# Kernel tuning notes

Measured on AMD Instinct MI355X. Metric: run time of the kernel, lower is better.

Reference implementation:

```python
import jax, jax.numpy as jnp
import numpy as np


def setup_inputs() -> dict:
    key = jax.random.key(0)
    ks = jax.random.split(key, 7)
    B, T, D_in, H, D_out = 512, 1024, 128, 512, 128
    s = lambda k, shp, fan: jax.random.normal(k, shp, jnp.float32) / np.sqrt(fan)
    return {
        "x": jax.random.normal(ks[0], (B, T, D_in), jnp.float32),
        "Wx": s(ks[1], (H, D_in), D_in),
        "bx": jnp.zeros((H,), jnp.float32),
        "Wh": s(ks[2], (H, H), H),
        "bh": jnp.zeros((H,), jnp.float32),
        "Wy": s(ks[3], (D_out, H), H),
        "by": jnp.zeros((D_out,), jnp.float32),
    }


def reference(x, Wx, bx, Wh, bh, Wy, by):
    # x: [B, T, D_in]. Hoist input projection into one big GEMM (same math).
    B, T, _ = x.shape
    H = Wh.shape[0]
    xp = jnp.einsum("btd,hd->bth", x, Wx) + bx + bh  # [B, T, H]

    def step(h, xp_t):
        h = jnp.tanh(xp_t + h @ Wh.T)
        return h, None

    h0 = jnp.zeros((B, H), x.dtype)
    h_T, _ = jax.lax.scan(step, h0, jnp.swapaxes(xp, 0, 1))  # scan over time
    y = h_T @ Wy.T + by  # [B, D_out]
    return y
```

## Files before the change

### kernel.cpp

```cpp
#include <hip/hip_runtime.h>

typedef __bf16 bf16x8 __attribute__((ext_vector_type(8)));
typedef unsigned short ushort8_t __attribute__((ext_vector_type(8)));
typedef float f32x4 __attribute__((ext_vector_type(4)));
typedef unsigned int uint4_t __attribute__((ext_vector_type(4)));

#define MFMA16(a,b,c) __builtin_amdgcn_mfma_f32_16x16x32_bf16((a),(b),(c),0,0,0)


__device__ __forceinline__ unsigned short f2bf(float f) {
  unsigned int u = __float_as_uint(f);
  u += 0x7FFFu + ((u >> 16) & 1u);
  return (unsigned short)(u >> 16);
}

__device__ __forceinline__ bf16x8 pack8(const float* __restrict__ s) {
  ushort8_t u;
#pragma unroll
  for (int j = 0; j < 8; ++j) u[j] = f2bf(s[j]);
  return __builtin_bit_cast(bf16x8, u);
}

__global__ void rnn_prep(const float* __restrict__ Wx, const float* __restrict__ bx,
                         const float* __restrict__ Wh, const float* __restrict__ bh,
                         void* __restrict__ ws) {
  int gid = blockIdx.x * 256 + threadIdx.x;
  if (blockIdx.x < 72) {
    int l = gid & 63;
    int f = (gid >> 6) % 18;
    int w = gid / (64 * 18);
    int nt = f & 1, fi = f >> 1;
    int n = w * 32 + nt * 16 + (l & 15);
    int kg = l >> 4;
    const float* src;
    if (fi < 5) src = Wh + (size_t)n * 512 + (11 + fi) * 32 + kg * 8;
    else        src = Wx + (size_t)n * 128 + (fi - 5) * 32 + kg * 8;
    ushort8_t u;
#pragma unroll
    for (int j = 0; j < 8; ++j) u[j] = f2bf(src[j]);
    ((ushort8_t*)ws)[gid] = u;
  } else {
    int i = (gid - 72 * 256) * 2;
    float* bias = (float*)((char*)ws + 294912);
    bias[i]     = bx[i] + bh[i];
    bias[i + 1] = bx[i + 1] + bh[i + 1];
  }
}

__global__ __launch_bounds__(1024) void rnn_scan(
    const float* __restrict__ x, const float* __restrict__ Wh,
    const float* __restrict__ Wy, const float* __restrict__ by,
    const void* __restrict__ ws, float* __restrict__ out) {
  __shared__ alignas(16) char h_lds[32768];
  __shared__ alignas(16) char x_lds[8192];

  const int tid = threadIdx.x;
  const int w = tid >> 6, l = tid & 63;
  const int m = l & 15, kg = l >> 4;
  const int sw = (m & 7) << 4;
  const int bb = blockIdx.x << 4;

  const int hE = m * 1024 + ((kg * 16) ^ sw);
  const int hO = m * 1024 + ((64 + kg * 16) ^ sw);
  const int xE = m * 256 + ((kg * 16) ^ sw);
  const int xO = m * 256 + ((64 + kg * 16) ^ sw);

  const float* xrow = x + (size_t)(bb + w) * (1024 * 128) + 2 * l;
  const int k2 = 2 * l;
  const int xw_off = w * 256 + ((k2 >> 6) << 7) + ((2 * (k2 & 63)) ^ ((w & 7) << 4));

  int cblk[2], ca2[2];
#pragma unroll
  for (int nt = 0; nt < 2; ++nt) {
    int c = w * 32 + nt * 16 + m;
    cblk[nt] = (c >> 6) << 7;
    ca2[nt] = 2 * (c & 63);
  }

  const float* bias = (const float*)((const char*)ws + 294912);
  const float b0 = bias[w * 32 + m];
  const float b1 = bias[w * 32 + 16 + m];

  bf16x8 bres[22];
#pragma unroll
  for (int kt = 0; kt < 11; ++kt)
#pragma unroll
    for (int nt = 0; nt < 2; ++nt)
      bres[kt * 2 + nt] = pack8(Wh + (size_t)(w * 32 + nt * 16 + m) * 512 + kt * 32 + kg * 8);

  const bf16x8* sp = (const bf16x8*)ws + (w * 18) * 64 + l;

  *(uint4_t*)(h_lds + tid * 16) = (uint4_t){0, 0, 0, 0};
  {
    float2 xv = *(const float2*)(xrow);
    unsigned int p = (unsigned)f2bf(xv.x) | ((unsigned)f2bf(xv.y) << 16);
    *(unsigned int*)(x_lds + xw_off) = p;
  }
  __syncthreads();

  for (int t = 0; t < 1024; ++t) {
    const int cur = t & 1, nxt = cur ^ 1;
    const char* hb = h_lds + cur * 16384;
    const char* xb = x_lds + cur * 4096;

    unsigned long long spi = (unsigned long long)sp;
    asm volatile("" : "+v"(spi));
    const bf16x8* spv = (const bf16x8*)spi;

    const int tt = (t < 1023) ? t + 1 : 1023;
    float2 xv = *(const float2*)(xrow + (size_t)tt * 128);

    f32x4 acc0 = {0.f, 0.f, 0.f, 0.f}, acc1 = {0.f, 0.f, 0.f, 0.f};

#pragma unroll
    for (int kt = 0; kt < 11; ++kt) {
      bf16x8 a = *(const bf16x8*)(hb + ((kt & 1) ? hO : hE) + (kt >> 1) * 128);
      acc0 = MFMA16(a, bres[kt * 2], acc0);
      acc1 = MFMA16(a, bres[kt * 2 + 1], acc1);
    }
#pragma unroll
    for (int fi = 0; fi < 9; ++fi) {
      const int kt = 11 + fi;
      bf16x8 sb0 = spv[(fi * 2) * 64];
      bf16x8 sb1 = spv[(fi * 2 + 1) * 64];
      bf16x8 a;
      if (kt < 16) {
        a = *(const bf16x8*)(hb + ((kt & 1) ? hO : hE) + (kt >> 1) * 128);
      } else {
        const int kx = kt - 16;
        a = *(const bf16x8*)(xb + ((kx & 1) ? xO : xE) + (kx >> 1) * 128);
      }
      acc0 = MFMA16(a, sb0, acc0);
      acc1 = MFMA16(a, sb1, acc1);
    }

    {
      unsigned int p = (unsigned)f2bf(xv.x) | ((unsigned)f2bf(xv.y) << 16);
      *(unsigned int*)(x_lds + nxt * 4096 + xw_off) = p;
    }

    char* hn = h_lds + nxt * 16384;
#pragma unroll
    for (int nt = 0; nt < 2; ++nt) {
      const float bnt = nt ? b1 : b0;
      const f32x4 av = nt ? acc1 : acc0;
#pragma unroll
      for (int i = 0; i < 4; ++i) {
        const int r = kg * 4 + i;
        float pre = av[i] + bnt;
        float e = __expf(2.f * pre);
        float hv = 1.f - 2.f / (e + 1.f);
        const int off = r * 1024 + cblk[nt] + (ca2[nt] ^ ((r & 7) << 4));
        *(unsigned short*)(hn + off) = f2bf(hv);
      }
    }
    __syncthreads();
  }

  if (w < 8) {
    f32x4 aY = {0.f, 0.f, 0.f, 0.f};
#pragma unroll
    for (int kt = 0; kt < 16; ++kt) {
      bf16x8 a = *(const bf16x8*)(h_lds + ((kt & 1) ? hO : hE) + (kt >> 1) * 128);
      bf16x8 b = pack8(Wy + (size_t)(w * 16 + m) * 512 + kt * 32 + kg * 8);
      aY = MFMA16(a, b, aY);
    }
    const float bv = by[w * 16 + m];
#pragma unroll
    for (int i = 0; i < 4; ++i)
      out[(size_t)(bb + kg * 4 + i) * 128 + w * 16 + m] = aY[i] + bv;
  }
}

extern "C" void kernel_launch(void* const* d_in, const int* in_sizes, int n_in,
                              void* d_out, int out_size, void* d_ws, size_t ws_size,
                              hipStream_t stream) {
  const float* x  = (const float*)d_in[0];
  const float* Wx = (const float*)d_in[1];
  const float* bx = (const float*)d_in[2];
  const float* Wh = (const float*)d_in[3];
  const float* bh = (const float*)d_in[4];
  const float* Wy = (const float*)d_in[5];
  const float* by = (const float*)d_in[6];

  rnn_prep<<<73, 256, 0, stream>>>(Wx, bx, Wh, bh, d_ws);
  rnn_scan<<<32, 1024, 0, stream>>>(x, Wh, Wy, by, d_ws, (float*)d_out);
}
```

Measured before the change: 5.133 ms.

## Split each batch group across two cooperating blocks exchanging hidden state via global mailboxes

After: 9.162 ms. 78.5% more time.

```diff
diff --git a/kernel.cpp b/kernel.cpp
--- a/kernel.cpp
+++ b/kernel.cpp
@@ -13,162 +13,204 @@
   u += 0x7FFFu + ((u >> 16) & 1u);
   return (unsigned short)(u >> 16);
 }
-
-__device__ __forceinline__ bf16x8 pack8(const float* __restrict__ s) {
+__device__ __forceinline__ bf16x8 pack8v(float4 a, float4 b) {
   ushort8_t u;
-#pragma unroll
-  for (int j = 0; j < 8; ++j) u[j] = f2bf(s[j]);
+  u[0] = f2bf(a.x); u[1] = f2bf(a.y); u[2] = f2bf(a.z); u[3] = f2bf(a.w);
+  u[4] = f2bf(b.x); u[5] = f2bf(b.y); u[6] = f2bf(b.z); u[7] = f2bf(b.w);
   return __builtin_bit_cast(bf16x8, u);
 }
-
-__global__ void rnn_prep(const float* __restrict__ Wx, const float* __restrict__ bx,
-                         const float* __restrict__ Wh, const float* __restrict__ bh,
+__device__ __forceinline__ bf16x8 pack8p(const float* __restrict__ s) {
+  float4 a = *(const float4*)s, b = *(const float4*)(s + 4);
+  return pack8v(a, b);
+}
+
+__global__ void rnn_prep(const float* __restrict__ bx, const float* __restrict__ bh,
                          void* __restrict__ ws) {
-  int gid = blockIdx.x * 256 + threadIdx.x;
-  if (blockIdx.x < 72) {
-    int l = gid & 63;
-    int f = (gid >> 6) % 18;
-    int w = gid / (64 * 18);
-    int nt = f & 1, fi = f >> 1;
-    int n = w * 32 + nt * 16 + (l & 15);
-    int kg = l >> 4;
-    const float* src;
-    if (fi < 5) src = Wh + (size_t)n * 512 + (11 + fi) * 32 + kg * 8;
-    else        src = Wx + (size_t)n * 128 + (fi - 5) * 32 + kg * 8;
-    ushort8_t u;
-#pragma unroll
-    for (int j = 0; j < 8; ++j) u[j] = f2bf(src[j]);
-    ((ushort8_t*)ws)[gid] = u;
-  } else {
-    int i = (gid - 72 * 256) * 2;
-    float* bias = (float*)((char*)ws + 294912);
-    bias[i]     = bx[i] + bh[i];
-    bias[i + 1] = bx[i + 1] + bh[i + 1];
-  }
-}
-
-__global__ __launch_bounds__(1024) void rnn_scan(
-    const float* __restrict__ x, const float* __restrict__ Wh,
-    const float* __restrict__ Wy, const float* __restrict__ by,
-    const void* __restrict__ ws, float* __restrict__ out) {
+  int tid = threadIdx.x;
+  ((float*)ws)[tid] = bx[tid] + bh[tid];
+  if (tid < 128) *(unsigned*)((char*)ws + 2048 + tid * 64) = 0u;
+}
+
+__global__ __launch_bounds__(256, 1) void rnn_scan(
+    const float* __restrict__ x, const float* __restrict__ Wx,
+    const float* __restrict__ Wh, const float* __restrict__ Wy,
+    const float* __restrict__ by, void* __restrict__ ws,
+    float* __restrict__ out) {
   __shared__ alignas(16) char h_lds[32768];
   __shared__ alignas(16) char x_lds[8192];
 
   const int tid = threadIdx.x;
-  const int w = tid >> 6, l = tid & 63;
-  const int m = l & 15, kg = l >> 4;
+  const int w = tid >> 6, l = tid & 63, m = l & 15, kg = l >> 4;
+  const int g = blockIdx.x & 31, role = blockIdx.x >> 5;
+  const int bb = g << 4;
+  const int pbase = (1 - role) << 8;
   const int sw = (m & 7) << 4;
-  const int bb = blockIdx.x << 4;
-
-  const int hE = m * 1024 + ((kg * 16) ^ sw);
-  const int hO = m * 1024 + ((64 + kg * 16) ^ sw);
-  const int xE = m * 256 + ((kg * 16) ^ sw);
-  const int xO = m * 256 + ((64 + kg * 16) ^ sw);
-
-  const float* xrow = x + (size_t)(bb + w) * (1024 * 128) + 2 * l;
-  const int k2 = 2 * l;
-  const int xw_off = w * 256 + ((k2 >> 6) << 7) + ((2 * (k2 & 63)) ^ ((w & 7) << 4));
-
-  int cblk[2], ca2[2];
-#pragma unroll
-  for (int nt = 0; nt < 2; ++nt) {
-    int c = w * 32 + nt * 16 + m;
-    cblk[nt] = (c >> 6) << 7;
-    ca2[nt] = 2 * (c & 63);
-  }
-
-  const float* bias = (const float*)((const char*)ws + 294912);
-  const float b0 = bias[w * 32 + m];
-  const float b1 = bias[w * 32 + 16 + m];
-
-  bf16x8 bres[22];
-#pragma unroll
-  for (int kt = 0; kt < 11; ++kt)
-#pragma unroll
-    for (int nt = 0; nt < 2; ++nt)
-      bres[kt * 2 + nt] = pack8(Wh + (size_t)(w * 32 + nt * 16 + m) * 512 + kt * 32 + kg * 8);
-
-  const bf16x8* sp = (const bf16x8*)ws + (w * 18) * 64 + l;
-
-  *(uint4_t*)(h_lds + tid * 16) = (uint4_t){0, 0, 0, 0};
+
+  char* wsb = (char*)ws;
+  const float* biasp = (const float*)wsb;
+
+  bf16x8 bw[20][4];
+  float bv[4];
+#pragma unroll
+  for (int nt = 0; nt < 4; ++nt) {
+    const int cn = role * 256 + w * 64 + nt * 16 + m;
+    bv[nt] = biasp[cn];
+#pragma unroll
+    for (int kt = 0; kt < 16; ++kt)
+      bw[kt][nt] = pack8p(Wh + (size_t)cn * 512 + kt * 32 + kg * 8);
+#pragma unroll
+    for (int kx = 0; kx < 4; ++kx)
+      bw[16 + kx][nt] = pack8p(Wx + (size_t)cn * 128 + kx * 32 + kg * 8);
+  }
+
+  int aoff_h[16], aoff_x[4];
+#pragma unroll
+  for (int kt = 0; kt < 16; ++kt)
+    aoff_h[kt] = m * 1024 + ((kt >> 1) << 7) + ((((kt & 1) << 6) + (kg << 4)) ^ sw);
+#pragma unroll
+  for (int kx = 0; kx < 4; ++kx)
+    aoff_x[kx] = m * 256 + ((kx >> 1) << 7) + ((((kx & 1) << 6) + (kg << 4)) ^ sw);
+
+  const int srow = tid >> 4, sk0 = (tid & 15) << 3;
+  const float* xsrc = x + (size_t)(bb + srow) * 1024 * 128 + sk0;
+  const int xw_off = srow * 256 + ((sk0 >> 6) << 7) + (((sk0 & 63) << 1) ^ ((srow & 7) << 4));
+
+  char* const mail_my0 = wsb + 16384 + (size_t)((g * 2 + role) * 2 + 0) * 8192;
+  char* const mail_my1 = wsb + 16384 + (size_t)((g * 2 + role) * 2 + 1) * 8192;
+  const char* const mail_pt0 = wsb + 16384 + (size_t)((g * 2 + (1 - role)) * 2 + 0) * 8192;
+  const char* const mail_pt1 = wsb + 16384 + (size_t)((g * 2 + (1 - role)) * 2 + 1) * 8192;
+  unsigned* const flag_my0 = (unsigned*)(wsb + 2048 + ((g * 2 + role) * 2 + 0) * 64);
+  unsigned* const flag_my1 = (unsigned*)(wsb + 2048 + ((g * 2 + role) * 2 + 1) * 64);
+  const unsigned* const flag_pt0 = (const unsigned*)(wsb + 2048 + ((g * 2 + (1 - role)) * 2 + 0) * 64);
+  const unsigned* const flag_pt1 = (const unsigned*)(wsb + 2048 + ((g * 2 + (1 - role)) * 2 + 1) * 64);
+
   {
-    float2 xv = *(const float2*)(xrow);
-    unsigned int p = (unsigned)f2bf(xv.x) | ((unsigned)f2bf(xv.y) << 16);
-    *(unsigned int*)(x_lds + xw_off) = p;
+    uint4_t z = {0, 0, 0, 0};
+#pragma unroll
+    for (int j = 0; j < 4; ++j) *(uint4_t*)(h_lds + tid * 64 + j * 16) = z;
+    float4 xa = *(const float4*)(xsrc);
+    float4 xb2 = *(const float4*)(xsrc + 4);
+    *(bf16x8*)(x_lds + xw_off) = pack8v(xa, xb2);
   }
   __syncthreads();
 
   for (int t = 0; t < 1024; ++t) {
-    const int cur = t & 1, nxt = cur ^ 1;
-    const char* hb = h_lds + cur * 16384;
-    const char* xb = x_lds + cur * 4096;
-
-    unsigned long long spi = (unsigned long long)sp;
-    asm volatile("" : "+v"(spi));
-    const bf16x8* spv = (const bf16x8*)spi;
+    const int cur = t & 1;
+    const int par = (t + 1) & 1;
+    const char* hb = h_lds + (cur << 14);
+    const char* xbuf = x_lds + (cur << 12);
+    char* hn = h_lds + ((cur ^ 1) << 14);
+    char* xn = x_lds + ((cur ^ 1) << 12);
+    char* mm = par ? mail_my1 : mail_my0;
+    const char* mp = par ? mail_pt1 : mail_pt0;
+    unsigned* fm = par ? flag_my1 : flag_my0;
+    const unsigned* fp = par ? flag_pt1 : flag_pt0;
 
     const int tt = (t < 1023) ? t + 1 : 1023;
-    float2 xv = *(const float2*)(xrow + (size_t)tt * 128);
-
-    f32x4 acc0 = {0.f, 0.f, 0.f, 0.f}, acc1 = {0.f, 0.f, 0.f, 0.f};
-
-#pragma unroll
-    for (int kt = 0; kt < 11; ++kt) {
-      bf16x8 a = *(const bf16x8*)(hb + ((kt & 1) ? hO : hE) + (kt >> 1) * 128);
-      acc0 = MFMA16(a, bres[kt * 2], acc0);
-      acc1 = MFMA16(a, bres[kt * 2 + 1], acc1);
-    }
-#pragma unroll
-    for (int fi = 0; fi < 9; ++fi) {
-      const int kt = 11 + fi;
-      bf16x8 sb0 = spv[(fi * 2) * 64];
-      bf16x8 sb1 = spv[(fi * 2 + 1) * 64];
-      bf16x8 a;
-      if (kt < 16) {
-        a = *(const bf16x8*)(hb + ((kt & 1) ? hO : hE) + (kt >> 1) * 128);
-      } else {
-        const int kx = kt - 16;
-        a = *(const bf16x8*)(xb + ((kx & 1) ? xO : xE) + (kx >> 1) * 128);
+    float4 xa = *(const float4*)(xsrc + (size_t)tt * 128);
+    float4 xb2 = *(const float4*)(xsrc + (size_t)tt * 128 + 4);
+
+    f32x4 a0 = {0, 0, 0, 0}, a1 = {0, 0, 0, 0}, a2 = {0, 0, 0, 0}, a3 = {0, 0, 0, 0};
+#pragma unroll
+    for (int kt = 0; kt < 16; ++kt) {
+      bf16x8 a = *(const bf16x8*)(hb + aoff_h[kt]);
+      a0 = MFMA16(a, bw[kt][0], a0);
+      a1 = MFMA16(a, bw[kt][1], a1);
+      a2 = MFMA16(a, bw[kt][2], a2);
+      a3 = MFMA16(a, bw[kt][3], a3);
+    }
+#pragma unroll
+    for (int kx = 0; kx < 4; ++kx) {
+      bf16x8 a = *(const bf16x8*)(xbuf + aoff_x[kx]);
+      a0 = MFMA16(a, bw[16 + kx][0], a0);
+      a1 = MFMA16(a, bw[16 + kx][1], a1);
+      a2 = MFMA16(a, bw[16 + kx][2], a2);
+      a3 = MFMA16(a, bw[16 + kx][3], a3);
+    }
+
+    unsigned pk[4][2];
+#pragma unroll
+    for (int ct = 0; ct < 4; ++ct) {
+      const f32x4 av = ct == 0 ? a0 : ct == 1 ? a1 : ct == 2 ? a2 : a3;
+      unsigned short hv[4];
+#pragma unroll
+      for (int i = 0; i < 4; ++i) {
+        float pre = av[i] + bv[ct];
+        float e = __expf(2.f * pre);
+        hv[i] = f2bf(1.f - 2.f / (e + 1.f));
       }
-      acc0 = MFMA16(a, sb0, acc0);
-      acc1 = MFMA16(a, sb1, acc1);
-    }
-
-    {
-      unsigned int p = (unsigned)f2bf(xv.x) | ((unsigned)f2bf(xv.y) << 16);
-      *(unsigned int*)(x_lds + nxt * 4096 + xw_off) = p;
-    }
-
-    char* hn = h_lds + nxt * 16384;
-#pragma unroll
-    for (int nt = 0; nt < 2; ++nt) {
-      const float bnt = nt ? b1 : b0;
-      const f32x4 av = nt ? acc1 : acc0;
+      pk[ct][0] = (unsigned)hv[0] | ((unsigned)hv[1] << 16);
+      pk[ct][1] = (unsigned)hv[2] | ((unsigned)hv[3] << 16);
+    }
+
+#pragma unroll
+    for (int ct = 0; ct < 4; ++ct) {
+      unsigned* dst = (unsigned*)(mm + (w * 64 + ct * 16 + m) * 32 + kg * 8);
+      __hip_atomic_store(dst, pk[ct][0], __ATOMIC_RELAXED, __HIP_MEMORY_SCOPE_AGENT);
+      __hip_atomic_store(dst + 1, pk[ct][1], __ATOMIC_RELAXED, __HIP_MEMORY_SCOPE_AGENT);
+    }
+    __syncthreads();
+    if (tid == 0) {
+      __threadfence();
+      __hip_atomic_store(fm, (unsigned)(t + 1), __ATOMIC_RELEASE, __HIP_MEMORY_SCOPE_AGENT);
+    }
+
+#pragma unroll
+    for (int ct = 0; ct < 4; ++ct) {
 #pragma unroll
       for (int i = 0; i < 4; ++i) {
         const int r = kg * 4 + i;
-        float pre = av[i] + bnt;
-        float e = __expf(2.f * pre);
-        float hv = 1.f - 2.f / (e + 1.f);
-        const int off = r * 1024 + cblk[nt] + (ca2[nt] ^ ((r & 7) << 4));
-        *(unsigned short*)(hn + off) = f2bf(hv);
+        const int off = r * 1024 + ((role * 4 + w) << 7) + ((ct * 32 + 2 * m) ^ ((r & 7) << 4));
+        const unsigned v = (i & 1) ? (pk[ct][i >> 1] >> 16) : (pk[ct][i >> 1] & 0xffffu);
+        *(unsigned short*)(hn + off) = (unsigned short)v;
       }
     }
+    *(bf16x8*)(xn + xw_off) = pack8v(xa, xb2);
+
+    if (l == 0) {
+      while (__hip_atomic_load(fp, __ATOMIC_RELAXED, __HIP_MEMORY_SCOPE_AGENT) < (unsigned)(t + 1)) {}
+    }
+    __threadfence();
+
+    {
+      const unsigned* src = (const unsigned*)(mp + tid * 32);
+      unsigned d[8];
+#pragma unroll
+      for (int j = 0; j < 8; ++j)
+        d[j] = __hip_atomic_load(src + j, __ATOMIC_RELAXED, __HIP_MEMORY_SCOPE_AGENT);
+      const int k = pbase + tid;
+      const int kb = ((k >> 6) << 7);
+      const int k2 = 2 * (k & 63);
+#pragma unroll
+      for (int j = 0; j < 8; ++j) {
+#pragma unroll
+        for (int h2 = 0; h2 < 2; ++h2) {
+          const int r = 2 * j + h2;
+          const int off = r * 1024 + kb + (k2 ^ ((r & 7) << 4));
+          const unsigned short v = h2 ? (unsigned short)(d[j] >> 16) : (unsigned short)(d[j] & 0xffffu);
+          *(unsigned short*)(hn + off) = v;
+        }
+      }
+    }
     __syncthreads();
   }
 
-  if (w < 8) {
-    f32x4 aY = {0.f, 0.f, 0.f, 0.f};
+  if (role == 0) {
+    f32x4 y0 = {0, 0, 0, 0}, y1 = {0, 0, 0, 0};
+    const int c0 = w * 32 + m, c1 = w * 32 + 16 + m;
 #pragma unroll
     for (int kt = 0; kt < 16; ++kt) {
-      bf16x8 a = *(const bf16x8*)(h_lds + ((kt & 1) ? hO : hE) + (kt >> 1) * 128);
-      bf16x8 b = pack8(Wy + (size_t)(w * 16 + m) * 512 + kt * 32 + kg * 8);
-      aY = MFMA16(a, b, aY);
-    }
-    const float bv = by[w * 16 + m];
-#pragma unroll
-    for (int i = 0; i < 4; ++i)
-      out[(size_t)(bb + kg * 4 + i) * 128 + w * 16 + m] = aY[i] + bv;
+      bf16x8 a = *(const bf16x8*)(h_lds + aoff_h[kt]);
+      y0 = MFMA16(a, pack8p(Wy + (size_t)c0 * 512 + kt * 32 + kg * 8), y0);
+      y1 = MFMA16(a, pack8p(Wy + (size_t)c1 * 512 + kt * 32 + kg * 8), y1);
+    }
+    const float b0 = by[c0], b1 = by[c1];
+#pragma unroll
+    for (int i = 0; i < 4; ++i) {
+      const int r = kg * 4 + i;
+      out[(size_t)(bb + r) * 128 + c0] = y0[i] + b0;
+      out[(size_t)(bb + r) * 128 + c1] = y1[i] + b1;
+    }
   }
 }
 
@@ -183,6 +225,6 @@
   const float* Wy = (const float*)d_in[5];
   const float* by = (const float*)d_in[6];
 
-  rnn_prep<<<73, 256, 0, stream>>>(Wx, bx, Wh, bh, d_ws);
-  rnn_scan<<<32, 1024, 0, stream>>>(x, Wh, Wy, by, d_ws, (float*)d_out);
-}
+  rnn_prep<<<1, 512, 0, stream>>>(bx, bh, d_ws);
+  rnn_scan<<<64, 256, 0, stream>>>(x, Wx, Wh, Wy, by, d_ws, (float*)d_out);
+}
```
